# Optimization experiments

Measured on AMD Instinct MI355X. Metric: run time of the kernel, lower is better.

## Reference

```python
import jax, jax.numpy as jnp
import numpy as np

N_NODES = 2708  # hardcoded dim_size in the original aggregate()
IN_C = 2048
OUT_C = 512
N_EDGES = 500000


def setup_inputs() -> dict:
    key = jax.random.key(0)
    k1, k2, k3, k4 = jax.random.split(key, 4)
    x = jax.random.normal(k1, (N_NODES, IN_C), dtype=jnp.float32)
    edge_index = jax.random.randint(k2, (2, N_EDGES), 0, N_NODES, dtype=jnp.int32)
    weight = jax.random.normal(k3, (OUT_C, IN_C), dtype=jnp.float32) * (1.0 / np.sqrt(IN_C))
    bias = jax.random.normal(k4, (OUT_C,), dtype=jnp.float32) * 0.01
    return {"x": x, "edge_index": edge_index, "weight": weight, "bias": bias}


def reference(x, edge_index, weight, bias):
    # Dropout omitted (eval-mode equivalent; p=0.5 only active in training).
    # F.linear: y = x @ W^T + b  -> [N, OUT_C]
    h = jnp.einsum('ni,oi->no', x, weight) + bias
    # message: gather source-node features per edge  -> [E, OUT_C]
    msgs = h[edge_index[0]]
    # aggregate: scatter_add into destination nodes (fixed dim_size=2708)
    out = jax.ops.segment_sum(msgs, edge_index[1], num_segments=N_NODES)
    return out
```

## Files before the change

### kernel.cpp

```cpp
#include <hip/hip_runtime.h>
#include <stdint.h>

typedef unsigned short u16;
typedef unsigned int u32;

#define N_NODES 2708
#define IN_C    2048
#define OUT_C   512
#define MP      2816
#define KP      2816

using floatx4 = __attribute__((ext_vector_type(4))) float;
using short8  = __attribute__((ext_vector_type(8))) short;

constexpr size_t XB_OFF = 0;
constexpr size_t XB_SZ  = (size_t)MP * IN_C * 2;
constexpr size_t WB_OFF = XB_OFF + XB_SZ;
constexpr size_t WB_SZ  = (size_t)OUT_C * IN_C * 2;
constexpr size_t HT_OFF = WB_OFF + WB_SZ;
constexpr size_t HT_SZ  = (size_t)OUT_C * MP * 2;
constexpr size_t AC_OFF = HT_OFF + HT_SZ;
constexpr size_t AC_SZ  = (size_t)MP * KP * 2;
constexpr size_t P_OFF  = AC_OFF + AC_SZ;
constexpr size_t P_SZ   = (size_t)2 * OUT_C * MP * 4;

constexpr int ZF4 = (int)(AC_SZ / 16);
constexpr int GEMM_BLK = 704;

static __device__ __forceinline__ u16 f2bf(float f) {
  union { float f; u32 u; } v; v.f = f;
  u32 r = v.u + 0x7fffu + ((v.u >> 16) & 1u);
  return (u16)(r >> 16);
}
static __device__ __forceinline__ u32 cvt2(u32 w) {
  float lo = (float)(w & 0xffffu), hi = (float)(w >> 16);
  return (u32)f2bf(lo) | ((u32)f2bf(hi) << 16);
}

constexpr int XBLK = MP * IN_C / 8 / 256;
constexpr int WBLK = OUT_C * IN_C / 8 / 256;
constexpr int ZBLK = ZF4 / 256;
constexpr int PREP_BLK = XBLK + WBLK + ZBLK;

__global__ void k_prep(const float* __restrict__ x, const float* __restrict__ w,
                       u16* __restrict__ xb, u16* __restrict__ wb,
                       float4* __restrict__ zac) {
  const int b = blockIdx.x, tid = threadIdx.x;
  if (b < XBLK) {
    const int i = b * 256 + tid;
    const int row = i >> 8, col = (i & 255) * 8;
    union { u16 u[8]; uint4 v; } o;
    if (row < N_NODES) {
      float4 v0 = *(const float4*)&x[(size_t)row * IN_C + col];
      float4 v1 = *(const float4*)&x[(size_t)row * IN_C + col + 4];
      o.u[0]=f2bf(v0.x); o.u[1]=f2bf(v0.y); o.u[2]=f2bf(v0.z); o.u[3]=f2bf(v0.w);
      o.u[4]=f2bf(v1.x); o.u[5]=f2bf(v1.y); o.u[6]=f2bf(v1.z); o.u[7]=f2bf(v1.w);
    } else {
      o.v = make_uint4(0, 0, 0, 0);
    }
    *(uint4*)&xb[(size_t)row * IN_C + col] = o.v;
  } else if (b < XBLK + WBLK) {
    const int idx = ((b - XBLK) * 256 + tid) * 8;
    float4 v0 = *(const float4*)&w[idx];
    float4 v1 = *(const float4*)&w[idx + 4];
    union { u16 u[8]; uint4 v; } o;
    o.u[0]=f2bf(v0.x); o.u[1]=f2bf(v0.y); o.u[2]=f2bf(v0.z); o.u[3]=f2bf(v0.w);
    o.u[4]=f2bf(v1.x); o.u[5]=f2bf(v1.y); o.u[6]=f2bf(v1.z); o.u[7]=f2bf(v1.w);
    *(uint4*)&wb[idx] = o.v;
  } else {
    zac[(b - XBLK - WBLK) * 256 + tid] = make_float4(0.f, 0.f, 0.f, 0.f);
  }
}

__global__ void k_count(const int* __restrict__ ei, u32* __restrict__ Ac, int E) {
  int e = blockIdx.x * 256 + threadIdx.x;
  if (e < E) {
    int src = ei[e];
    int dst = ei[E + e];
    u32 idx = (u32)dst * KP + (u32)src;
    atomicAdd(&Ac[idx >> 1], 1u << ((idx & 1) * 16));
  }
}

__global__ void k_cvtA(uint4* __restrict__ A, int n) {
  int i = blockIdx.x * 256 + threadIdx.x;
  if (i < n) {
    uint4 v = A[i];
    A[i] = make_uint4(cvt2(v.x), cvt2(v.y), cvt2(v.z), cvt2(v.w));
  }
}

template<int LDK, int NKI, int EPI>
__global__ __launch_bounds__(256, 3) void k_gemm(
    const u16* __restrict__ A, const u16* __restrict__ B, float* __restrict__ dst) {
  __shared__ u16 lA[3][64 * 64];
  __shared__ u16 lB[3][64 * 64];
  const int tid = threadIdx.x, lane = tid & 63, wid = tid >> 6;

  const int cpx = (int)gridDim.x >> 3;
  const int orig = blockIdx.x;
  const int swz = (orig & 7) * cpx + (orig >> 3);
  const int bn = swz & 7;
  const int rest = swz >> 3;
  const int ks = (rest >= 44) ? 1 : 0;
  const int bm = rest - ks * 44;
  const int bmr = bm * 64, bnr = bn * 64;
  const long k0b = (long)ks * LDK;

  const int wr = wid >> 1, wc = wid & 1;

  const int swzl = ((lane & 7) ^ ((lane >> 3) & 7)) * 16;
  const char* ag[2];
  const char* bg[2];
#pragma unroll
  for (int j = 0; j < 2; ++j) {
    int c = wid + 4 * j, row = 8 * c + (lane >> 3);
    ag[j] = (const char*)A + (size_t)(bmr + row) * (LDK * 2) + k0b + swzl;
    bg[j] = (const char*)B + (size_t)(bnr + row) * (LDK * 2) + k0b + swzl;
  }

#define STAGE(bb, tt) do {                                                        \
  _Pragma("unroll")                                                               \
  for (int j = 0; j < 2; ++j) {                                                   \
    __builtin_amdgcn_global_load_lds(                                             \
      (const __attribute__((address_space(1))) u32*)(ag[j] + (size_t)(tt) * 128), \
      (__attribute__((address_space(3))) u32*)&lA[bb][(wid + 4 * j) * 512],       \
      16, 0, 0);                                                                  \
    __builtin_amdgcn_global_load_lds(                                             \
      (const __attribute__((address_space(1))) u32*)(bg[j] + (size_t)(tt) * 128), \
      (__attribute__((address_space(3))) u32*)&lB[bb][(wid + 4 * j) * 512],       \
      16, 0, 0);                                                                  \
  }                                                                               \
} while (0)

  floatx4 acc[2][2] = {};

  STAGE(0, 0);
  if (NKI > 1) STAGE(1, 1);
  int cur = 0;
  for (int t = 0; t < NKI; ++t) {
    if (t + 1 < NKI) asm volatile("s_waitcnt vmcnt(4)" ::: "memory");
    else             asm volatile("s_waitcnt vmcnt(0)" ::: "memory");
    __builtin_amdgcn_s_barrier();
    asm volatile("" ::: "memory");
    if (t + 2 < NKI) {
      int nb = cur + 2; if (nb >= 3) nb -= 3;
      STAGE(nb, t + 2);
    }
    const u16* pA = lA[cur];
    const u16* pB = lB[cur];
    short8 af[2][2], bf[2][2];
#pragma unroll
    for (int mi = 0; mi < 2; ++mi)
#pragma unroll
      for (int kk = 0; kk < 2; ++kk) {
        const int row = wr * 32 + mi * 16 + (lane & 15);
        const int col8 = ((kk * 4 + (lane >> 4)) ^ (lane & 7)) * 8;
        af[mi][kk] = *(const short8*)&pA[row * 64 + col8];
      }
#pragma unroll
    for (int ni = 0; ni < 2; ++ni)
#pragma unroll
      for (int kk = 0; kk < 2; ++kk) {
        const int row = wc * 32 + ni * 16 + (lane & 15);
        const int col8 = ((kk * 4 + (lane >> 4)) ^ (lane & 7)) * 8;
        bf[ni][kk] = *(const short8*)&pB[row * 64 + col8];
      }
    __builtin_amdgcn_s_setprio(1);
#pragma unroll
    for (int kk = 0; kk < 2; ++kk)
#pragma unroll
      for (int mi = 0; mi < 2; ++mi)
#pragma unroll
        for (int ni = 0; ni < 2; ++ni)
          acc[mi][ni] = __builtin_amdgcn_mfma_f32_16x16x32_bf16(af[mi][kk], bf[ni][kk], acc[mi][ni], 0, 0, 0);
    __builtin_amdgcn_s_setprio(0);
    ++cur; if (cur >= 3) cur -= 3;
  }
#undef STAGE

  const int lr = (lane >> 4) * 4, lc = lane & 15;
  if (EPI == 0) {
#pragma unroll
    for (int ni = 0; ni < 2; ++ni) {
      const int n = bnr + wc * 32 + ni * 16 + lc;
#pragma unroll
      for (int mi = 0; mi < 2; ++mi) {
        const int m0 = bmr + wr * 32 + mi * 16 + lr;
        *(floatx4*)&dst[((size_t)ks * OUT_C + n) * MP + m0] = acc[mi][ni];
      }
    }
  } else {
#pragma unroll
    for (int mi = 0; mi < 2; ++mi)
#pragma unroll
      for (int j = 0; j < 4; ++j) {
        const int m = bmr + wr * 32 + mi * 16 + lr + j;
#pragma unroll
        for (int ni = 0; ni < 2; ++ni) {
          const int n = bnr + wc * 32 + ni * 16 + lc;
          dst[((size_t)ks * MP + m) * OUT_C + n] = acc[mi][ni][j];
        }
      }
  }
}

__global__ void k_red1(const float* __restrict__ P1, const float* __restrict__ bias,
                       u16* __restrict__ hT) {
  int i8 = blockIdx.x * 256 + threadIdx.x;
  int n = i8 / (MP / 8);
  int m0 = (i8 - n * (MP / 8)) * 8;
  float bv = bias[n];
  const float* p0 = &P1[(size_t)n * MP + m0];
  const float* p1 = p0 + (size_t)OUT_C * MP;
  float4 a0 = *(const float4*)p0, a1 = *(const float4*)(p0 + 4);
  float4 b0 = *(const float4*)p1, b1 = *(const float4*)(p1 + 4);
  union { u16 u[8]; uint4 v; } o;
  o.u[0]=f2bf(a0.x+b0.x+bv); o.u[1]=f2bf(a0.y+b0.y+bv);
  o.u[2]=f2bf(a0.z+b0.z+bv); o.u[3]=f2bf(a0.w+b0.w+bv);
  o.u[4]=f2bf(a1.x+b1.x+bv); o.u[5]=f2bf(a1.y+b1.y+bv);
  o.u[6]=f2bf(a1.z+b1.z+bv); o.u[7]=f2bf(a1.w+b1.w+bv);
  *(uint4*)&hT[(size_t)n * MP + m0] = o.v;
}

__global__ void k_red2(const float* __restrict__ P2, float* __restrict__ out) {
  int i = blockIdx.x * 256 + threadIdx.x;
  size_t o = (size_t)i * 4;
  float4 a = *(const float4*)&P2[o];
  float4 b = *(const float4*)&P2[(size_t)MP * OUT_C + o];
  *(float4*)&out[o] = make_float4(a.x + b.x, a.y + b.y, a.z + b.z, a.w + b.w);
}

extern "C" void kernel_launch(void* const* d_in, const int* in_sizes, int n_in,
                              void* d_out, int out_size, void* d_ws, size_t ws_size,
                              hipStream_t stream) {
  const float* x    = (const float*)d_in[0];
  const int*   ei   = (const int*)d_in[1];
  const float* w    = (const float*)d_in[2];
  const float* bias = (const float*)d_in[3];
  float* out = (float*)d_out;

  char* ws = (char*)d_ws;
  u16*   xb = (u16*)(ws + XB_OFF);
  u16*   wb = (u16*)(ws + WB_OFF);
  u16*   hT = (u16*)(ws + HT_OFF);
  u16*   Ac = (u16*)(ws + AC_OFF);
  float* P  = (float*)(ws + P_OFF);

  const int E = in_sizes[1] / 2;

  k_prep<<<dim3(PREP_BLK), dim3(256), 0, stream>>>(x, w, xb, wb, (float4*)Ac);
  k_count<<<dim3((E + 255) / 256), dim3(256), 0, stream>>>(ei, (u32*)Ac, E);
  k_cvtA<<<dim3(ZF4 / 256), dim3(256), 0, stream>>>((uint4*)Ac, ZF4);
  k_gemm<IN_C, IN_C / 2 / 64, 0><<<dim3(GEMM_BLK), dim3(256), 0, stream>>>(xb, wb, P);
  k_red1<<<dim3(OUT_C * MP / 8 / 256), dim3(256), 0, stream>>>(P, bias, hT);
  k_gemm<KP, KP / 2 / 64, 1><<<dim3(GEMM_BLK), dim3(256), 0, stream>>>(Ac, hT, P);
  k_red2<<<dim3(N_NODES * OUT_C / 4 / 256), dim3(256), 0, stream>>>(P, out);
}
```

Measured before the change: 142.6 us.

## Use 8-bit edge counts and fuse count-to-bf16 conversion into first GEMM

Edge multiplicities are now counted into a byte-packed buffer instead of 16-bit slots, which halves the memory the zeroing and atomic passes touch. The separate conversion kernel is removed. Extra trailing blocks in the first GEMM launch expand the byte counts into a new bf16 adjacency buffer, overlapping that conversion with the GEMM tiles. The swizzle now hardcodes 88 blocks per column group because gridDim grew. The risk is count overflow if any (dst,src) pair has more than 255 edges, and a larger workspace.

```diff
diff --git a/kernel.cpp b/kernel.cpp
--- a/kernel.cpp
+++ b/kernel.cpp
@@ -1,6 +1,7 @@
 #include <hip/hip_runtime.h>
 #include <stdint.h>
 
+typedef unsigned char  u8;
 typedef unsigned short u16;
 typedef unsigned int u32;
 
@@ -13,38 +14,37 @@
 using floatx4 = __attribute__((ext_vector_type(4))) float;
 using short8  = __attribute__((ext_vector_type(8))) short;
 
-constexpr size_t XB_OFF = 0;
-constexpr size_t XB_SZ  = (size_t)MP * IN_C * 2;
-constexpr size_t WB_OFF = XB_OFF + XB_SZ;
-constexpr size_t WB_SZ  = (size_t)OUT_C * IN_C * 2;
-constexpr size_t HT_OFF = WB_OFF + WB_SZ;
-constexpr size_t HT_SZ  = (size_t)OUT_C * MP * 2;
-constexpr size_t AC_OFF = HT_OFF + HT_SZ;
-constexpr size_t AC_SZ  = (size_t)MP * KP * 2;
-constexpr size_t P_OFF  = AC_OFF + AC_SZ;
-constexpr size_t P_SZ   = (size_t)2 * OUT_C * MP * 4;
-
-constexpr int ZF4 = (int)(AC_SZ / 16);
+constexpr size_t XB_OFF  = 0;
+constexpr size_t XB_SZ   = (size_t)MP * IN_C * 2;
+constexpr size_t WB_OFF  = XB_OFF + XB_SZ;
+constexpr size_t WB_SZ   = (size_t)OUT_C * IN_C * 2;
+constexpr size_t HT_OFF  = WB_OFF + WB_SZ;
+constexpr size_t HT_SZ   = (size_t)OUT_C * MP * 2;
+constexpr size_t CNT_OFF = HT_OFF + HT_SZ;
+constexpr size_t CNT_SZ  = (size_t)MP * KP;
+constexpr size_t AB_OFF  = CNT_OFF + CNT_SZ;
+constexpr size_t AB_SZ   = (size_t)MP * KP * 2;
+constexpr size_t P_OFF   = AB_OFF + AB_SZ;
+constexpr size_t P_SZ    = (size_t)2 * OUT_C * MP * 4;
+
 constexpr int GEMM_BLK = 704;
+constexpr int CVT_I4   = (int)(CNT_SZ / 16);
+constexpr int CVT_BLK  = CVT_I4 / 256;
 
 static __device__ __forceinline__ u16 f2bf(float f) {
   union { float f; u32 u; } v; v.f = f;
   u32 r = v.u + 0x7fffu + ((v.u >> 16) & 1u);
   return (u16)(r >> 16);
 }
-static __device__ __forceinline__ u32 cvt2(u32 w) {
-  float lo = (float)(w & 0xffffu), hi = (float)(w >> 16);
-  return (u32)f2bf(lo) | ((u32)f2bf(hi) << 16);
-}
 
 constexpr int XBLK = MP * IN_C / 8 / 256;
 constexpr int WBLK = OUT_C * IN_C / 8 / 256;
-constexpr int ZBLK = ZF4 / 256;
+constexpr int ZBLK = CVT_I4 / 256;
 constexpr int PREP_BLK = XBLK + WBLK + ZBLK;
 
 __global__ void k_prep(const float* __restrict__ x, const float* __restrict__ w,
                        u16* __restrict__ xb, u16* __restrict__ wb,
-                       float4* __restrict__ zac) {
+                       uint4* __restrict__ zcnt) {
   const int b = blockIdx.x, tid = threadIdx.x;
   if (b < XBLK) {
     const int i = b * 256 + tid;
@@ -68,38 +68,46 @@
     o.u[4]=f2bf(v1.x); o.u[5]=f2bf(v1.y); o.u[6]=f2bf(v1.z); o.u[7]=f2bf(v1.w);
     *(uint4*)&wb[idx] = o.v;
   } else {
-    zac[(b - XBLK - WBLK) * 256 + tid] = make_float4(0.f, 0.f, 0.f, 0.f);
-  }
-}
-
-__global__ void k_count(const int* __restrict__ ei, u32* __restrict__ Ac, int E) {
+    zcnt[(b - XBLK - WBLK) * 256 + tid] = make_uint4(0, 0, 0, 0);
+  }
+}
+
+__global__ void k_count(const int* __restrict__ ei, u32* __restrict__ Cnt, int E) {
   int e = blockIdx.x * 256 + threadIdx.x;
   if (e < E) {
     int src = ei[e];
     int dst = ei[E + e];
     u32 idx = (u32)dst * KP + (u32)src;
-    atomicAdd(&Ac[idx >> 1], 1u << ((idx & 1) * 16));
-  }
-}
-
-__global__ void k_cvtA(uint4* __restrict__ A, int n) {
-  int i = blockIdx.x * 256 + threadIdx.x;
-  if (i < n) {
-    uint4 v = A[i];
-    A[i] = make_uint4(cvt2(v.x), cvt2(v.y), cvt2(v.z), cvt2(v.w));
-  }
-}
-
-template<int LDK, int NKI, int EPI>
+    atomicAdd(&Cnt[idx >> 2], 1u << ((idx & 3) * 8));
+  }
+}
+
+template<int LDK, int NKI, int EPI, bool FUSECVT>
 __global__ __launch_bounds__(256, 3) void k_gemm(
-    const u16* __restrict__ A, const u16* __restrict__ B, float* __restrict__ dst) {
+    const u16* __restrict__ A, const u16* __restrict__ B, float* __restrict__ dst,
+    const uint4* __restrict__ Cnt, u16* __restrict__ Ab) {
+  const int tid = threadIdx.x;
+  if (FUSECVT && blockIdx.x >= GEMM_BLK) {
+    const int i = (blockIdx.x - GEMM_BLK) * 256 + tid;
+    uint4 v = Cnt[i];
+    union { u16 u[16]; uint4 q[2]; } o;
+    const u32 wv[4] = { v.x, v.y, v.z, v.w };
+#pragma unroll
+    for (int j = 0; j < 4; ++j)
+#pragma unroll
+      for (int bq = 0; bq < 4; ++bq)
+        o.u[j * 4 + bq] = f2bf((float)((wv[j] >> (bq * 8)) & 0xffu));
+    uint4* dstq = (uint4*)&Ab[(size_t)i * 16];
+    dstq[0] = o.q[0];
+    dstq[1] = o.q[1];
+    return;
+  }
   __shared__ u16 lA[3][64 * 64];
   __shared__ u16 lB[3][64 * 64];
-  const int tid = threadIdx.x, lane = tid & 63, wid = tid >> 6;
-
-  const int cpx = (int)gridDim.x >> 3;
+  const int lane = tid & 63, wid = tid >> 6;
+
   const int orig = blockIdx.x;
-  const int swz = (orig & 7) * cpx + (orig >> 3);
+  const int swz = (orig & 7) * 88 + (orig >> 3);
   const int bn = swz & 7;
   const int rest = swz >> 3;
   const int ks = (rest >= 44) ? 1 : 0;
@@ -241,19 +249,22 @@
   float* out = (float*)d_out;
 
   char* ws = (char*)d_ws;
-  u16*   xb = (u16*)(ws + XB_OFF);
-  u16*   wb = (u16*)(ws + WB_OFF);
-  u16*   hT = (u16*)(ws + HT_OFF);
-  u16*   Ac = (u16*)(ws + AC_OFF);
-  float* P  = (float*)(ws + P_OFF);
+  u16*   xb  = (u16*)(ws + XB_OFF);
+  u16*   wb  = (u16*)(ws + WB_OFF);
+  u16*   hT  = (u16*)(ws + HT_OFF);
+  u8*    Cnt = (u8*)(ws + CNT_OFF);
+  u16*   Ab  = (u16*)(ws + AB_OFF);
+  float* P   = (float*)(ws + P_OFF);
 
   const int E = in_sizes[1] / 2;
 
-  k_prep<<<dim3(PREP_BLK), dim3(256), 0, stream>>>(x, w, xb, wb, (float4*)Ac);
-  k_count<<<dim3((E + 255) / 256), dim3(256), 0, stream>>>(ei, (u32*)Ac, E);
-  k_cvtA<<<dim3(ZF4 / 256), dim3(256), 0, stream>>>((uint4*)Ac, ZF4);
-  k_gemm<IN_C, IN_C / 2 / 64, 0><<<dim3(GEMM_BLK), dim3(256), 0, stream>>>(xb, wb, P);
+  k_prep<<<dim3(PREP_BLK), dim3(256), 0, stream>>>(x, w, xb, wb, (uint4*)Cnt);
+  k_count<<<dim3((E + 255) / 256), dim3(256), 0, stream>>>(ei, (u32*)Cnt, E);
+  k_gemm<IN_C, IN_C / 2 / 64, 0, true>
+      <<<dim3(GEMM_BLK + CVT_BLK), dim3(256), 0, stream>>>(
+          xb, wb, P, (const uint4*)Cnt, Ab);
   k_red1<<<dim3(OUT_C * MP / 8 / 256), dim3(256), 0, stream>>>(P, bias, hT);
-  k_gemm<KP, KP / 2 / 64, 1><<<dim3(GEMM_BLK), dim3(256), 0, stream>>>(Ac, hT, P);
+  k_gemm<KP, KP / 2 / 64, 1, false>
+      <<<dim3(GEMM_BLK), dim3(256), 0, stream>>>(Ab, hT, P, nullptr, nullptr);
   k_red2<<<dim3(N_NODES * OUT_C / 4 / 256), dim3(256), 0, stream>>>(P, out);
 }
```

Result: faster. 136.4 us (-4.4%).
